# Optimization experiments

Hardware: AMD Instinct MI355X
Metric: run time of the kernel (lower is better)

Reference implementation:

```python
import jax, jax.numpy as jnp
import numpy as np

D = 64
H = 4
L = 3
T = 10
SEQ_OUT = 5
B = 16384
EPS = 1e-5


def setup_inputs() -> dict:
    key = jax.random.key(0)
    ks = iter(jax.random.split(key, 32))
    nrm = lambda shape, s: (jax.random.normal(next(ks), shape, jnp.float32) * s)
    inp = {
        'x': jax.random.normal(next(ks), (B, T, 4), jnp.float32),
        'embed_w': nrm((4, D), 0.5),
        'embed_b': jnp.zeros((D,), jnp.float32),
        'ln1_g': jnp.ones((L, D), jnp.float32),
        'ln1_b': jnp.zeros((L, D), jnp.float32),
        'qkv_w': nrm((L, D, 3 * D), D ** -0.5),
        'proj_w': nrm((L, D, D), D ** -0.5),
        'ln2_g': jnp.ones((L, D), jnp.float32),
        'ln2_b': jnp.zeros((L, D), jnp.float32),
        'ffn_w1': nrm((L, D, 4 * D), D ** -0.5),
        'ffn_b1': jnp.zeros((L, 4 * D), jnp.float32),
        'ffn_w2': nrm((L, 4 * D, D), (4 * D) ** -0.5),
        'ffn_b2': jnp.zeros((L, D), jnp.float32),
        'lnf_g': jnp.ones((D,), jnp.float32),
        'lnf_b': jnp.zeros((D,), jnp.float32),
        'head_w': nrm((D, 2 * SEQ_OUT), D ** -0.5),
        'head_b': jnp.zeros((2 * SEQ_OUT,), jnp.float32),
    }
    return inp


def _layer_norm(x, g, b):
    m = jnp.mean(x, axis=-1, keepdims=True)
    v = jnp.mean((x - m) ** 2, axis=-1, keepdims=True)
    return (x - m) * jax.lax.rsqrt(v + EPS) * g + b


def _attention(x, qkv_w, proj_w):
    Bc, Tc, C = x.shape
    dh = C // H
    qkv = x @ qkv_w                      # [B,T,3C]
    q, k, v = jnp.split(qkv, 3, axis=-1)
    q = q.reshape(Bc, Tc, H, dh)
    k = k.reshape(Bc, Tc, H, dh)
    v = v.reshape(Bc, Tc, H, dh)
    att = jnp.einsum('bqhd,bkhd->bhqk', q, k) * (dh ** -0.5)
    mask = jnp.triu(jnp.ones((Tc, Tc), bool), 1)  # strictly upper
    att = jnp.where(mask, jnp.float32(-1e9), att)
    att = jax.nn.softmax(att, axis=-1)
    y = jnp.einsum('bhqk,bkhd->bqhd', att, v).reshape(Bc, Tc, C)
    return y @ proj_w


def reference(x, embed_w, embed_b, ln1_g, ln1_b, qkv_w, proj_w, ln2_g, ln2_b,
              ffn_w1, ffn_b1, ffn_w2, ffn_b2, lnf_g, lnf_b, head_w, head_b):
    h = x @ embed_w + embed_b
    for i in range(L):
        h = h + _attention(_layer_norm(h, ln1_g[i], ln1_b[i]), qkv_w[i], proj_w[i])
        z = _layer_norm(h, ln2_g[i], ln2_b[i])
        z = jax.nn.gelu(z @ ffn_w1[i] + ffn_b1[i], approximate=False)
        h = h + (z @ ffn_w2[i] + ffn_b2[i])
    h = _layer_norm(h, lnf_g, lnf_b)
    out = h[:, -1, :] @ head_w + head_b
    return out.reshape(-1, SEQ_OUT, 2)
```

## Files before the change

### kernel.cpp

```cpp
#include <hip/hip_runtime.h>

namespace {

typedef __bf16 bf16x8 __attribute__((ext_vector_type(8)));
typedef float f32x4 __attribute__((ext_vector_type(4)));

constexpr int NB = 8;
constexpr int ROWS = 80;
constexpr int MT = 5;
constexpr int APAD = 72;
constexpr int TPITCH = 82;
constexpr int NBLK = 16384 / NB;
constexpr float EPS = 1e-5f;

constexpr int PROJF_OFF = 36864;
constexpr int F1F_OFF = 49152;
constexpr int F2F_OFF = 98304;
constexpr int WS_ELEMS = 147456;

constexpr int ACT_OFF = 0;
constexpr int BUFQ_OFF = 11520;
constexpr int BUFK_OFF = 23040;
constexpr int SPR_OFF = 34560;
constexpr int ARENA_BYTES = 40960;

__device__ __forceinline__ uint pk2(float lo, float hi) {
  ushort ul = __builtin_bit_cast(ushort, (__bf16)lo);
  ushort uh = __builtin_bit_cast(ushort, (__bf16)hi);
  return (uint)ul | ((uint)uh << 16);
}
__device__ __forceinline__ void unpack8(int4 v, float* f) {
  uint u;
  u = (uint)v.x; f[0] = __uint_as_float(u << 16); f[1] = __uint_as_float(u & 0xffff0000u);
  u = (uint)v.y; f[2] = __uint_as_float(u << 16); f[3] = __uint_as_float(u & 0xffff0000u);
  u = (uint)v.z; f[4] = __uint_as_float(u << 16); f[5] = __uint_as_float(u & 0xffff0000u);
  u = (uint)v.w; f[6] = __uint_as_float(u << 16); f[7] = __uint_as_float(u & 0xffff0000u);
}
__device__ __forceinline__ float gelu_f(float v) {
  float ax = fabsf(v) * 0.70710678118f;
  float t = __builtin_amdgcn_rcpf(fmaf(0.3275911f, ax, 1.0f));
  float poly = t * fmaf(t, fmaf(t, fmaf(t, fmaf(t, 1.061405429f, -1.453152027f),
                                        1.421413741f), -0.284496736f), 0.254829592f);
  float erfv = fmaf(-poly, __expf(-ax * ax), 1.0f);
  erfv = copysignf(erfv, v);
  return 0.5f * v * (1.0f + erfv);
}
__device__ __forceinline__ f32x4 mfma_bf16(int4 a, int4 b, f32x4 c) {
  return __builtin_amdgcn_mfma_f32_16x16x32_bf16(
      __builtin_bit_cast(bf16x8, a), __builtin_bit_cast(bf16x8, b), c, 0, 0, 0);
}

__global__ __launch_bounds__(256) void prep_weights(
    const float* __restrict__ qkv_w, const float* __restrict__ proj_w,
    const float* __restrict__ ffn_w1, const float* __restrict__ ffn_w2,
    __bf16* __restrict__ ws) {
  int idx = blockIdx.x * 256 + threadIdx.x;
  if (idx >= WS_ELEMS) return;
  const float* src;
  int N, Ksz, lstride, base;
  if (idx < PROJF_OFF) { src = qkv_w; N = 192; Ksz = 64; lstride = 12288; base = idx; }
  else if (idx < F1F_OFF) { src = proj_w; N = 64; Ksz = 64; lstride = 4096; base = idx - PROJF_OFF; }
  else if (idx < F2F_OFF) { src = ffn_w1; N = 256; Ksz = 64; lstride = 16384; base = idx - F1F_OFF; }
  else { src = ffn_w2; N = 64; Ksz = 256; lstride = 16384; base = idx - F2F_OFF; }
  int layer = base / lstride, rem = base % lstride;
  int ntk = N / 16;
  int kt = rem / (ntk * 512); rem %= (ntk * 512);
  int nt = rem / 512;
  int lane = (rem % 512) / 8, j = rem % 8;
  int k = kt * 32 + (lane >> 4) * 8 + j;
  int n = nt * 16 + (lane & 15);
  ws[idx] = (__bf16)src[(size_t)layer * Ksz * N + (size_t)k * N + n];
}

__global__ __launch_bounds__(256, 4) void wtf_mfma(
    const float* __restrict__ x, const float* __restrict__ embed_w,
    const float* __restrict__ embed_b, const float* __restrict__ ln1_g,
    const float* __restrict__ ln1_b, const float* __restrict__ ln2_g,
    const float* __restrict__ ln2_b, const float* __restrict__ ffn_b1,
    const float* __restrict__ ffn_b2, const float* __restrict__ lnf_g,
    const float* __restrict__ lnf_b, const float* __restrict__ head_w,
    const float* __restrict__ head_b, const __bf16* __restrict__ wf,
    float* __restrict__ out) {
  const int tid = threadIdx.x;
  const int lane = tid & 63;
  const int w = tid >> 6;
  const int li16 = lane & 15;
  const int lg = lane >> 4;
  const int col = w * 16 + li16;

  __shared__ __align__(16) char lds_arena[ARENA_BYTES];
  __bf16(*actA)[APAD] = (__bf16(*)[APAD])(lds_arena + ACT_OFF);
  __bf16(*bufQ)[APAD] = (__bf16(*)[APAD])(lds_arena + BUFQ_OFF);
  __bf16(*bufK)[APAD] = (__bf16(*)[APAD])(lds_arena + BUFK_OFF);
  __bf16* bufT        = (__bf16*)(lds_arena + ACT_OFF);
  float(*hscr)[66]    = (float(*)[66])(lds_arena + BUFQ_OFF);
  __bf16* sP          = (__bf16*)(lds_arena + SPR_OFF);
  float* sXf          = (float*)(lds_arena + SPR_OFF);
  float2(*sPart)[3]   = (float2(*)[3])(lds_arena + SPR_OFF);
  float* sGB          = (float*)(lds_arena + SPR_OFF + 2048);

  f32x4 h[MT];

  auto ln_reg = [&](const float* g, const float* b) {
#pragma unroll
    for (int mt = 0; mt < MT; ++mt)
#pragma unroll
      for (int r = 0; r < 4; ++r) hscr[mt * 16 + lg * 4 + r][col] = h[mt][r];
    if (tid < 64) { sGB[tid] = g[tid]; sGB[64 + tid] = b[tid]; }
    __syncthreads();
    const int row = tid % 80;
    const int c3 = tid / 80;
    const int beg = (c3 == 0) ? 0 : (c3 == 1) ? 22 : 44;
    const int len2 = (c3 < 2) ? 11 : 10;
    if (tid < 240) {
      float s = 0.f, s2 = 0.f;
      for (int k = 0; k < len2; ++k) {
        float2 v = *(const float2*)&hscr[row][beg + 2 * k];
        s += v.x + v.y;
        s2 = fmaf(v.x, v.x, fmaf(v.y, v.y, s2));
      }
      sPart[row][c3] = make_float2(s, s2);
    }
    __syncthreads();
    if (tid < 240) {
      float2 p0 = sPart[row][0], p1 = sPart[row][1], p2 = sPart[row][2];
      float s = p0.x + p1.x + p2.x, s2 = p0.y + p1.y + p2.y;
      float m = s * 0.015625f;
      float rstd = rsqrtf(s2 * 0.015625f - m * m + EPS);
      for (int k = 0; k < len2; ++k) {
        int c = beg + 2 * k;
        float2 v = *(const float2*)&hscr[row][c];
        float v0 = (v.x - m) * rstd * sGB[c] + sGB[64 + c];
        float v1 = (v.y - m) * rstd * sGB[c + 1] + sGB[64 + c + 1];
        *(uint*)&actA[row][c] = pk2(v0, v1);
      }
    }
    __syncthreads();
  };

  {
    const float* xb = x + (size_t)blockIdx.x * (NB * 40);
    sXf[tid] = xb[tid];
    if (tid < NB * 40 - 256) sXf[256 + tid] = xb[256 + tid];
  }
  __syncthreads();
  {
    float ew0 = embed_w[col], ew1 = embed_w[64 + col];
    float ew2 = embed_w[128 + col], ew3 = embed_w[192 + col];
    float eb = embed_b[col];
#pragma unroll
    for (int mt = 0; mt < MT; ++mt)
#pragma unroll
      for (int r = 0; r < 4; ++r) {
        int row = mt * 16 + lg * 4 + r;
        const float* xv = &sXf[(row & 7) * 40 + (row >> 3) * 4];
        float acc = eb;
        acc = fmaf(xv[0], ew0, acc);
        acc = fmaf(xv[1], ew1, acc);
        acc = fmaf(xv[2], ew2, acc);
        acc = fmaf(xv[3], ew3, acc);
        h[mt][r] = acc;
      }
  }
  __syncthreads();

  for (int li = 0; li < 3; ++li) {
    const __bf16* qf = wf + li * 12288;
    const __bf16* pf = wf + PROJF_OFF + li * 4096;
    const __bf16* f1 = wf + F1F_OFF + li * 16384;
    const __bf16* f2 = wf + F2F_OFF + li * 16384;

    ln_reg(&ln1_g[li * 64], &ln1_b[li * 64]);

    uint2 vpk[MT];
    {
      int4 bq[3][2];
#pragma unroll
      for (int ii = 0; ii < 3; ++ii)
#pragma unroll
        for (int kt = 0; kt < 2; ++kt)
          bq[ii][kt] = ((const int4*)qf)[(kt * 12 + (w + 4 * ii)) * 64 + lane];
#pragma unroll
      for (int mt = 0; mt < MT; ++mt) {
        int arow = mt * 16 + li16;
        int4 a0 = *(const int4*)&actA[arow][lg * 8];
        int4 a1 = *(const int4*)&actA[arow][32 + lg * 8];
        f32x4 aq = {0.f, 0.f, 0.f, 0.f};
        aq = mfma_bf16(a0, bq[0][0], aq);
        aq = mfma_bf16(a1, bq[0][1], aq);
#pragma unroll
        for (int r = 0; r < 4; ++r) bufQ[mt * 16 + lg * 4 + r][col] = (__bf16)aq[r];
        f32x4 ak = {0.f, 0.f, 0.f, 0.f};
        ak = mfma_bf16(a0, bq[1][0], ak);
        ak = mfma_bf16(a1, bq[1][1], ak);
#pragma unroll
        for (int r = 0; r < 4; ++r) bufK[mt * 16 + lg * 4 + r][col] = (__bf16)ak[r];
        f32x4 av = {0.f, 0.f, 0.f, 0.f};
        av = mfma_bf16(a0, bq[2][0], av);
        av = mfma_bf16(a1, bq[2][1], av);
        vpk[mt].x = pk2(av[0], av[1]);
        vpk[mt].y = pk2(av[2], av[3]);
      }
    }
    __syncthreads();

    {
      auto do_score = [&](int p) {
        int qt = 2 * p + (lane >> 5);
        int b = lane & 7, hh = (lane >> 3) & 3;
        float qv[16];
        {
          int4 qa = *(const int4*)&bufQ[qt * 8 + b][hh * 16];
          int4 qb = *(const int4*)&bufQ[qt * 8 + b][hh * 16 + 8];
          unpack8(qa, qv); unpack8(qb, qv + 8);
        }
        float sc[10], mx = -1e30f;
#pragma unroll
        for (int kt = 0; kt < 10; ++kt) {
          int4 ka = *(const int4*)&bufK[kt * 8 + b][hh * 16];
          int4 kb = *(const int4*)&bufK[kt * 8 + b][hh * 16 + 8];
          float kv[16]; unpack8(ka, kv); unpack8(kb, kv + 8);
          float d = 0.f;
#pragma unroll
          for (int i = 0; i < 16; ++i) d = fmaf(qv[i], kv[i], d);
          sc[kt] = (kt <= qt) ? d * 0.25f : -1e30f;
          mx = fmaxf(mx, sc[kt]);
        }
        float ssum = 0.f;
#pragma unroll
        for (int kt = 0; kt < 10; ++kt) { sc[kt] = __expf(sc[kt] - mx); ssum += sc[kt]; }
        float inv = __builtin_amdgcn_rcpf(ssum);
        __bf16* prow = &sP[((b * 4 + hh) * 10 + qt) * 10];
#pragma unroll
        for (int kt = 0; kt < 10; ++kt) prow[kt] = (__bf16)(sc[kt] * inv);
      };
      if (w == 0) { do_score(0); do_score(4); }
      else do_score(w);
      const int coff = col * TPITCH;
#pragma unroll
      for (int mt = 0; mt < MT; ++mt) {
        uint* dst = (uint*)&bufT[coff + mt * 16 + lg * 4];
        dst[0] = vpk[mt].x;
        dst[1] = vpk[mt].y;
      }
    }
    __syncthreads();

    {
      const int hh = lane >> 4;
      float vcol[2][10];
#pragma unroll
      for (int kt = 0; kt < 10; ++kt) {
        vcol[0][kt] = (float)bufT[lane * TPITCH + kt * 8 + w];
        vcol[1][kt] = (float)bufT[lane * TPITCH + kt * 8 + w + 4];
      }
#pragma unroll
      for (int it = 0; it < 20; ++it) {
        int r = w + 4 * it;
        int b = r & 7, qt = r >> 3, sel = it & 1;
        const __bf16* prow = &sP[((b * 4 + hh) * 10 + qt) * 10];
        float acc = 0.f;
#pragma unroll
        for (int kt = 0; kt < 10; ++kt)
          acc = fmaf((float)prow[kt], vcol[sel][kt], acc);
        bufK[r][lane] = (__bf16)acc;
      }
    }
    __syncthreads();

    {
      int4 b0 = ((const int4*)pf)[(0 * 4 + w) * 64 + lane];
      int4 b1 = ((const int4*)pf)[(1 * 4 + w) * 64 + lane];
#pragma unroll
      for (int mt = 0; mt < MT; ++mt) {
        int arow = mt * 16 + li16;
        int4 a0 = *(const int4*)&bufK[arow][lg * 8];
        int4 a1 = *(const int4*)&bufK[arow][32 + lg * 8];
        f32x4 acc = {0.f, 0.f, 0.f, 0.f};
        acc = mfma_bf16(a0, b0, acc);
        acc = mfma_bf16(a1, b1, acc);
#pragma unroll
        for (int r = 0; r < 4; ++r) h[mt][r] += acc[r];
      }
    }
    __syncthreads();

    ln_reg(&ln2_g[li * 64], &ln2_b[li * 64]);

    {
#pragma unroll
      for (int cp = 0; cp < 2; ++cp) {
#pragma unroll
        for (int cc = 0; cc < 2; ++cc) {
          int c = cp * 2 + cc;
          int nt1 = c * 4 + w;
          int4 b0 = ((const int4*)f1)[(0 * 16 + nt1) * 64 + lane];
          int4 b1 = ((const int4*)f1)[(1 * 16 + nt1) * 64 + lane];
          float bias1 = ffn_b1[li * 256 + c * 64 + col];
          __bf16(*gbuf)[APAD] = cc ? bufK : bufQ;
#pragma unroll
          for (int mt = 0; mt < MT; ++mt) {
            int arow = mt * 16 + li16;
            int4 a0 = *(const int4*)&actA[arow][lg * 8];
            int4 a1 = *(const int4*)&actA[arow][32 + lg * 8];
            f32x4 acc = {0.f, 0.f, 0.f, 0.f};
            acc = mfma_bf16(a0, b0, acc);
            acc = mfma_bf16(a1, b1, acc);
#pragma unroll
            for (int r = 0; r < 4; ++r)
              gbuf[mt * 16 + lg * 4 + r][col] = (__bf16)gelu_f(acc[r] + bias1);
          }
        }
        __syncthreads();
        f32x4 acc2[MT];
#pragma unroll
        for (int mt = 0; mt < MT; ++mt) acc2[mt] = {0.f, 0.f, 0.f, 0.f};
#pragma unroll
        for (int cc = 0; cc < 2; ++cc) {
          int c = cp * 2 + cc;
          int4 c0 = ((const int4*)f2)[((c * 2 + 0) * 4 + w) * 64 + lane];
          int4 c1 = ((const int4*)f2)[((c * 2 + 1) * 4 + w) * 64 + lane];
          __bf16(*gbuf)[APAD] = cc ? bufK : bufQ;
#pragma unroll
          for (int mt = 0; mt < MT; ++mt) {
            int arow = mt * 16 + li16;
            int4 a0 = *(const int4*)&gbuf[arow][lg * 8];
            int4 a1 = *(const int4*)&gbuf[arow][32 + lg * 8];
            acc2[mt] = mfma_bf16(a0, c0, acc2[mt]);
            acc2[mt] = mfma_bf16(a1, c1, acc2[mt]);
          }
        }
#pragma unroll
        for (int mt = 0; mt < MT; ++mt)
#pragma unroll
          for (int r = 0; r < 4; ++r) h[mt][r] += acc2[mt][r];
        __syncthreads();
      }
      float bias2 = ffn_b2[li * 64 + col];
#pragma unroll
      for (int mt = 0; mt < MT; ++mt)
#pragma unroll
        for (int r = 0; r < 4; ++r) h[mt][r] += bias2;
    }
  }

  if (lg >= 2) {
#pragma unroll
    for (int r = 0; r < 4; ++r) hscr[(lg - 2) * 4 + r][col] = h[4][r];
  }
  __syncthreads();
  float2* sFin = (float2*)(lds_arena + SPR_OFF);
  if (tid < 8) {
    float s = 0.f, s2 = 0.f;
#pragma unroll
    for (int i = 0; i < 64; ++i) { float v = hscr[tid][i]; s += v; s2 = fmaf(v, v, s2); }
    float m = s * 0.015625f;
    sFin[tid] = make_float2(m, rsqrtf(s2 * 0.015625f - m * m + EPS));
  }
  __syncthreads();
  if (tid < 80) {
    int b = tid / 10, j = tid % 10;
    float m = sFin[b].x, rstd = sFin[b].y;
    float acc = head_b[j];
#pragma unroll
    for (int d = 0; d < 64; ++d) {
      float z = (hscr[b][d] - m) * rstd * lnf_g[d] + lnf_b[d];
      acc = fmaf(z, head_w[d * 10 + j], acc);
    }
    out[((size_t)blockIdx.x * NB + b) * 10 + j] = acc;
  }
}

}

extern "C" void kernel_launch(void* const* d_in, const int* in_sizes, int n_in,
                              void* d_out, int out_size, void* d_ws, size_t ws_size,
                              hipStream_t stream) {
  const float* x       = (const float*)d_in[0];
  const float* embed_w = (const float*)d_in[1];
  const float* embed_b = (const float*)d_in[2];
  const float* ln1_g   = (const float*)d_in[3];
  const float* ln1_b   = (const float*)d_in[4];
  const float* qkv_w   = (const float*)d_in[5];
  const float* proj_w  = (const float*)d_in[6];
  const float* ln2_g   = (const float*)d_in[7];
  const float* ln2_b   = (const float*)d_in[8];
  const float* ffn_w1  = (const float*)d_in[9];
  const float* ffn_b1  = (const float*)d_in[10];
  const float* ffn_w2  = (const float*)d_in[11];
  const float* ffn_b2  = (const float*)d_in[12];
  const float* lnf_g   = (const float*)d_in[13];
  const float* lnf_b   = (const float*)d_in[14];
  const float* head_w  = (const float*)d_in[15];
  const float* head_b  = (const float*)d_in[16];
  __bf16* wf = (__bf16*)d_ws;
  float* out = (float*)d_out;

  prep_weights<<<dim3((WS_ELEMS + 255) / 256), dim3(256), 0, stream>>>(
      qkv_w, proj_w, ffn_w1, ffn_w2, wf);
  wtf_mfma<<<dim3(NBLK), dim3(256), 0, stream>>>(
      x, embed_w, embed_b, ln1_g, ln1_b, ln2_g, ln2_b, ffn_b1, ffn_b2,
      lnf_g, lnf_b, head_w, head_b, wf, out);
}
```

Measured before the change: 272.3 us.

## Shrink block to six sequences, pack 60 rows into four M-tiles, cheaper GELU

Each block now handles 6 sequences (60 rows) instead of 8 (80 rows), so the MFMA M-tiles drop from five to four, with the fourth tile only partly used and masked. LDS use goes down, and launch bounds move to 5 blocks per SM to raise occupancy. Causal attention scoring now runs one thread per (query, batch, head) and loops only over valid keys, and the P·V step reads packed probabilities. GELU changes from the erf polynomial to a tanh-form sigmoid approximation, which deviates from the exact-erf reference. Masking the partial tile wastes a quarter of that tile's MFMA work, and the grid needs a ragged tail guard.

```diff
diff --git a/kernel.cpp b/kernel.cpp
--- a/kernel.cpp
+++ b/kernel.cpp
@@ -5,12 +5,13 @@
 typedef __bf16 bf16x8 __attribute__((ext_vector_type(8)));
 typedef float f32x4 __attribute__((ext_vector_type(4)));
 
-constexpr int NB = 8;
-constexpr int ROWS = 80;
-constexpr int MT = 5;
+constexpr int NB = 6;
+constexpr int ROWS = 60;
+constexpr int MT = 4;
 constexpr int APAD = 72;
-constexpr int TPITCH = 82;
-constexpr int NBLK = 16384 / NB;
+constexpr int TPITCH = 62;
+constexpr int PPITCH = 12;
+constexpr int NBLK = (16384 + NB - 1) / NB;
 constexpr float EPS = 1e-5f;
 
 constexpr int PROJF_OFF = 36864;
@@ -19,31 +20,27 @@
 constexpr int WS_ELEMS = 147456;
 
 constexpr int ACT_OFF = 0;
-constexpr int BUFQ_OFF = 11520;
-constexpr int BUFK_OFF = 23040;
-constexpr int SPR_OFF = 34560;
-constexpr int ARENA_BYTES = 40960;
+constexpr int BUFQ_OFF = 8640;
+constexpr int BUFK_OFF = 17280;
+constexpr int SPR_OFF = 25920;
+constexpr int ARENA_BYTES = 31680;
 
 __device__ __forceinline__ uint pk2(float lo, float hi) {
   ushort ul = __builtin_bit_cast(ushort, (__bf16)lo);
   ushort uh = __builtin_bit_cast(ushort, (__bf16)hi);
   return (uint)ul | ((uint)uh << 16);
 }
+__device__ __forceinline__ float blo(uint u) { return __uint_as_float(u << 16); }
+__device__ __forceinline__ float bhi(uint u) { return __uint_as_float(u & 0xffff0000u); }
 __device__ __forceinline__ void unpack8(int4 v, float* f) {
-  uint u;
-  u = (uint)v.x; f[0] = __uint_as_float(u << 16); f[1] = __uint_as_float(u & 0xffff0000u);
-  u = (uint)v.y; f[2] = __uint_as_float(u << 16); f[3] = __uint_as_float(u & 0xffff0000u);
-  u = (uint)v.z; f[4] = __uint_as_float(u << 16); f[5] = __uint_as_float(u & 0xffff0000u);
-  u = (uint)v.w; f[6] = __uint_as_float(u << 16); f[7] = __uint_as_float(u & 0xffff0000u);
+  f[0] = blo(v.x); f[1] = bhi(v.x); f[2] = blo(v.y); f[3] = bhi(v.y);
+  f[4] = blo(v.z); f[5] = bhi(v.z); f[6] = blo(v.w); f[7] = bhi(v.w);
 }
 __device__ __forceinline__ float gelu_f(float v) {
-  float ax = fabsf(v) * 0.70710678118f;
-  float t = __builtin_amdgcn_rcpf(fmaf(0.3275911f, ax, 1.0f));
-  float poly = t * fmaf(t, fmaf(t, fmaf(t, fmaf(t, 1.061405429f, -1.453152027f),
-                                        1.421413741f), -0.284496736f), 0.254829592f);
-  float erfv = fmaf(-poly, __expf(-ax * ax), 1.0f);
-  erfv = copysignf(erfv, v);
-  return 0.5f * v * (1.0f + erfv);
+  float u = v * v;
+  float arg = v * fmaf(u, 0.0713548162f, 1.5957691216f);
+  float r = __builtin_amdgcn_rcpf(__expf(arg) + 1.0f);
+  return fmaf(-v, r, v);
 }
 __device__ __forceinline__ f32x4 mfma_bf16(int4 a, int4 b, f32x4 c) {
   return __builtin_amdgcn_mfma_f32_16x16x32_bf16(
@@ -72,7 +69,7 @@
   ws[idx] = (__bf16)src[(size_t)layer * Ksz * N + (size_t)k * N + n];
 }
 
-__global__ __launch_bounds__(256, 4) void wtf_mfma(
+__global__ __launch_bounds__(256, 5) void wtf_mfma(
     const float* __restrict__ x, const float* __restrict__ embed_w,
     const float* __restrict__ embed_b, const float* __restrict__ ln1_g,
     const float* __restrict__ ln1_b, const float* __restrict__ ln2_g,
@@ -108,11 +105,11 @@
       for (int r = 0; r < 4; ++r) hscr[mt * 16 + lg * 4 + r][col] = h[mt][r];
     if (tid < 64) { sGB[tid] = g[tid]; sGB[64 + tid] = b[tid]; }
     __syncthreads();
-    const int row = tid % 80;
-    const int c3 = tid / 80;
+    const int c3 = (tid >= 120) ? 2 : (tid >= 60 ? 1 : 0);
+    const int row = tid - c3 * 60;
     const int beg = (c3 == 0) ? 0 : (c3 == 1) ? 22 : 44;
     const int len2 = (c3 < 2) ? 11 : 10;
-    if (tid < 240) {
+    if (tid < 180) {
       float s = 0.f, s2 = 0.f;
       for (int k = 0; k < len2; ++k) {
         float2 v = *(const float2*)&hscr[row][beg + 2 * k];
@@ -122,7 +119,7 @@
       sPart[row][c3] = make_float2(s, s2);
     }
     __syncthreads();
-    if (tid < 240) {
+    if (tid < 180) {
       float2 p0 = sPart[row][0], p1 = sPart[row][1], p2 = sPart[row][2];
       float s = p0.x + p1.x + p2.x, s2 = p0.y + p1.y + p2.y;
       float m = s * 0.015625f;
@@ -139,9 +136,8 @@
   };
 
   {
-    const float* xb = x + (size_t)blockIdx.x * (NB * 40);
-    sXf[tid] = xb[tid];
-    if (tid < NB * 40 - 256) sXf[256 + tid] = xb[256 + tid];
+    int gx = blockIdx.x * (NB * 40) + tid;
+    if (tid < NB * 40 && gx < 16384 * 40) sXf[tid] = x[gx];
   }
   __syncthreads();
   {
@@ -153,7 +149,9 @@
 #pragma unroll
       for (int r = 0; r < 4; ++r) {
         int row = mt * 16 + lg * 4 + r;
-        const float* xv = &sXf[(row & 7) * 40 + (row >> 3) * 4];
+        int t = (row * 43691) >> 18;
+        int b = row - t * 6;
+        const float* xv = &sXf[b * 40 + t * 4];
         float acc = eb;
         acc = fmaf(xv[0], ew0, acc);
         acc = fmaf(xv[1], ew1, acc);
@@ -188,16 +186,18 @@
         f32x4 aq = {0.f, 0.f, 0.f, 0.f};
         aq = mfma_bf16(a0, bq[0][0], aq);
         aq = mfma_bf16(a1, bq[0][1], aq);
-#pragma unroll
-        for (int r = 0; r < 4; ++r) bufQ[mt * 16 + lg * 4 + r][col] = (__bf16)aq[r];
         f32x4 ak = {0.f, 0.f, 0.f, 0.f};
         ak = mfma_bf16(a0, bq[1][0], ak);
         ak = mfma_bf16(a1, bq[1][1], ak);
-#pragma unroll
-        for (int r = 0; r < 4; ++r) bufK[mt * 16 + lg * 4 + r][col] = (__bf16)ak[r];
         f32x4 av = {0.f, 0.f, 0.f, 0.f};
         av = mfma_bf16(a0, bq[2][0], av);
         av = mfma_bf16(a1, bq[2][1], av);
+        if (mt < MT - 1 || lg < 3) {
+#pragma unroll
+          for (int r = 0; r < 4; ++r) bufQ[mt * 16 + lg * 4 + r][col] = (__bf16)aq[r];
+#pragma unroll
+          for (int r = 0; r < 4; ++r) bufK[mt * 16 + lg * 4 + r][col] = (__bf16)ak[r];
+        }
         vpk[mt].x = pk2(av[0], av[1]);
         vpk[mt].y = pk2(av[2], av[3]);
       }
@@ -205,65 +205,86 @@
     __syncthreads();
 
     {
-      auto do_score = [&](int p) {
-        int qt = 2 * p + (lane >> 5);
-        int b = lane & 7, hh = (lane >> 3) & 3;
+      if (tid < 240) {
+        int qt = (tid * 43691) >> 20;
+        int bh = tid - qt * 24;
+        int b = bh >> 2, hh = bh & 3;
+        int qrow = qt * 6 + b;
         float qv[16];
         {
-          int4 qa = *(const int4*)&bufQ[qt * 8 + b][hh * 16];
-          int4 qb = *(const int4*)&bufQ[qt * 8 + b][hh * 16 + 8];
+          int4 qa = *(const int4*)&bufQ[qrow][hh * 16];
+          int4 qb = *(const int4*)&bufQ[qrow][hh * 16 + 8];
           unpack8(qa, qv); unpack8(qb, qv + 8);
         }
-        float sc[10], mx = -1e30f;
-#pragma unroll
-        for (int kt = 0; kt < 10; ++kt) {
-          int4 ka = *(const int4*)&bufK[kt * 8 + b][hh * 16];
-          int4 kb = *(const int4*)&bufK[kt * 8 + b][hh * 16 + 8];
+        float sc[10];
+#pragma unroll
+        for (int kt = 0; kt < 10; ++kt) sc[kt] = 0.f;
+        float mx = -1e30f;
+        for (int kt = 0; kt <= qt; ++kt) {
+          int4 ka = *(const int4*)&bufK[kt * 6 + b][hh * 16];
+          int4 kb = *(const int4*)&bufK[kt * 6 + b][hh * 16 + 8];
           float kv[16]; unpack8(ka, kv); unpack8(kb, kv + 8);
           float d = 0.f;
 #pragma unroll
           for (int i = 0; i < 16; ++i) d = fmaf(qv[i], kv[i], d);
-          sc[kt] = (kt <= qt) ? d * 0.25f : -1e30f;
-          mx = fmaxf(mx, sc[kt]);
+          d *= 0.25f;
+          sc[kt] = d;
+          mx = fmaxf(mx, d);
         }
         float ssum = 0.f;
-#pragma unroll
-        for (int kt = 0; kt < 10; ++kt) { sc[kt] = __expf(sc[kt] - mx); ssum += sc[kt]; }
+        for (int kt = 0; kt <= qt; ++kt) { sc[kt] = __expf(sc[kt] - mx); ssum += sc[kt]; }
         float inv = __builtin_amdgcn_rcpf(ssum);
-        __bf16* prow = &sP[((b * 4 + hh) * 10 + qt) * 10];
-#pragma unroll
-        for (int kt = 0; kt < 10; ++kt) prow[kt] = (__bf16)(sc[kt] * inv);
-      };
-      if (w == 0) { do_score(0); do_score(4); }
-      else do_score(w);
+        for (int kt = 0; kt <= qt; ++kt) sc[kt] *= inv;
+        __bf16* prow = &sP[(bh * 10 + qt) * PPITCH];
+#pragma unroll
+        for (int i = 0; i < 5; ++i)
+          *(uint*)&prow[2 * i] = pk2(sc[2 * i], sc[2 * i + 1]);
+      }
       const int coff = col * TPITCH;
 #pragma unroll
       for (int mt = 0; mt < MT; ++mt) {
-        uint* dst = (uint*)&bufT[coff + mt * 16 + lg * 4];
-        dst[0] = vpk[mt].x;
-        dst[1] = vpk[mt].y;
+        if (mt < MT - 1 || lg < 3) {
+          uint* dst = (uint*)&bufT[coff + mt * 16 + lg * 4];
+          dst[0] = vpk[mt].x;
+          dst[1] = vpk[mt].y;
+        }
       }
     }
     __syncthreads();
 
     {
       const int hh = lane >> 4;
-      float vcol[2][10];
+      const int b1 = (w + 4) % 6;
+      const int b2 = w + 2;
+      float vcol[3][10];
 #pragma unroll
       for (int kt = 0; kt < 10; ++kt) {
-        vcol[0][kt] = (float)bufT[lane * TPITCH + kt * 8 + w];
-        vcol[1][kt] = (float)bufT[lane * TPITCH + kt * 8 + w + 4];
-      }
-#pragma unroll
-      for (int it = 0; it < 20; ++it) {
-        int r = w + 4 * it;
-        int b = r & 7, qt = r >> 3, sel = it & 1;
-        const __bf16* prow = &sP[((b * 4 + hh) * 10 + qt) * 10];
+        vcol[0][kt] = (float)bufT[lane * TPITCH + kt * 6 + w];
+        vcol[1][kt] = (float)bufT[lane * TPITCH + kt * 6 + b1];
+        vcol[2][kt] = (float)bufT[lane * TPITCH + kt * 6 + b2];
+      }
+      int rb = w, rq = 0;
+#pragma unroll
+      for (int it = 0; it < 15; ++it) {
+        const int sel = it % 3;
+        const __bf16* prow = &sP[((rb * 4 + hh) * 10 + rq) * PPITCH];
+        uint2 pa = *(const uint2*)&prow[0];
+        uint2 pb = *(const uint2*)&prow[4];
+        uint pc = *(const uint*)&prow[8];
         float acc = 0.f;
-#pragma unroll
-        for (int kt = 0; kt < 10; ++kt)
-          acc = fmaf((float)prow[kt], vcol[sel][kt], acc);
-        bufK[r][lane] = (__bf16)acc;
+        acc = fmaf(blo(pa.x), vcol[sel][0], acc);
+        acc = fmaf(bhi(pa.x), vcol[sel][1], acc);
+        acc = fmaf(blo(pa.y), vcol[sel][2], acc);
+        acc = fmaf(bhi(pa.y), vcol[sel][3], acc);
+        acc = fmaf(blo(pb.x), vcol[sel][4], acc);
+        acc = fmaf(bhi(pb.x), vcol[sel][5], acc);
+        acc = fmaf(blo(pb.y), vcol[sel][6], acc);
+        acc = fmaf(bhi(pb.y), vcol[sel][7], acc);
+        acc = fmaf(blo(pc), vcol[sel][8], acc);
+        acc = fmaf(bhi(pc), vcol[sel][9], acc);
+        bufK[w + 4 * it][lane] = (__bf16)acc;
+        rb += 4;
+        if (rb >= 6) { rb -= 6; ++rq; }
       }
     }
     __syncthreads();
@@ -306,9 +327,11 @@
             f32x4 acc = {0.f, 0.f, 0.f, 0.f};
             acc = mfma_bf16(a0, b0, acc);
             acc = mfma_bf16(a1, b1, acc);
-#pragma unroll
-            for (int r = 0; r < 4; ++r)
-              gbuf[mt * 16 + lg * 4 + r][col] = (__bf16)gelu_f(acc[r] + bias1);
+            if (mt < MT - 1 || lg < 3) {
+#pragma unroll
+              for (int r = 0; r < 4; ++r)
+                gbuf[mt * 16 + lg * 4 + r][col] = (__bf16)gelu_f(acc[r] + bias1);
+            }
           }
         }
         __syncthreads();
@@ -344,13 +367,16 @@
     }
   }
 
-  if (lg >= 2) {
-#pragma unroll
-    for (int r = 0; r < 4; ++r) hscr[(lg - 2) * 4 + r][col] = h[4][r];
+  {
+#pragma unroll
+    for (int r = 0; r < 4; ++r) {
+      int row = 48 + lg * 4 + r;
+      if (row >= 54 && row < 60) hscr[row - 54][col] = h[3][r];
+    }
   }
   __syncthreads();
   float2* sFin = (float2*)(lds_arena + SPR_OFF);
-  if (tid < 8) {
+  if (tid < NB) {
     float s = 0.f, s2 = 0.f;
 #pragma unroll
     for (int i = 0; i < 64; ++i) { float v = hscr[tid][i]; s += v; s2 = fmaf(v, v, s2); }
@@ -358,16 +384,20 @@
     sFin[tid] = make_float2(m, rsqrtf(s2 * 0.015625f - m * m + EPS));
   }
   __syncthreads();
-  if (tid < 80) {
-    int b = tid / 10, j = tid % 10;
-    float m = sFin[b].x, rstd = sFin[b].y;
-    float acc = head_b[j];
-#pragma unroll
-    for (int d = 0; d < 64; ++d) {
-      float z = (hscr[b][d] - m) * rstd * lnf_g[d] + lnf_b[d];
-      acc = fmaf(z, head_w[d * 10 + j], acc);
-    }
-    out[((size_t)blockIdx.x * NB + b) * 10 + j] = acc;
+  if (tid < NB * 10) {
+    int b = (tid * 6554) >> 16;
+    int j = tid - b * 10;
+    int gb = blockIdx.x * NB + b;
+    if (gb < 16384) {
+      float m = sFin[b].x, rstd = sFin[b].y;
+      float acc = head_b[j];
+#pragma unroll
+      for (int d = 0; d < 64; ++d) {
+        float z = (hscr[b][d] - m) * rstd * lnf_g[d] + lnf_b[d];
+        acc = fmaf(z, head_w[d * 10 + j], acc);
+      }
+      out[(size_t)gb * 10 + j] = acc;
+    }
   }
 }
 
```

Measured after the change: 329.4 us. 21.0% more time.
